# Optimization experiments

Measured on AMD Instinct MI355X. Metric: run time of the kernel, lower is better.

The kernel has to match this reference:

```python
import jax, jax.numpy as jnp
import numpy as np

D = 768
H = 12
DH = 64
S = 1500
SCALE = 0.125  # 1/sqrt(64)


def setup_inputs() -> dict:
    key = jax.random.key(0)
    ks = jax.random.split(key, 8)
    def w(k):
        return jax.random.normal(k, (D, D), dtype=jnp.float32) * (1.0 / np.sqrt(D))
    x = jax.random.normal(ks[0], (8, S, D), dtype=jnp.float32)
    return {
        "x": x,
        "Wq": w(ks[1]), "bq": jax.random.normal(ks[2], (D,), dtype=jnp.float32) * 0.02,
        "Wk": w(ks[3]),
        "Wv": w(ks[4]), "bv": jax.random.normal(ks[5], (D,), dtype=jnp.float32) * 0.02,
        "Wo": w(ks[6]), "bo": jax.random.normal(ks[7], (D,), dtype=jnp.float32) * 0.02,
    }


def reference(x, Wq, bq, Wk, Wv, bv, Wo, bo):
    B = x.shape[0]
    # torch Linear: y = x @ W.T + b
    q = (jnp.einsum('bsd,ed->bse', x, Wq) + bq) * SCALE
    k = jnp.einsum('bsd,ed->bse', x, Wk)
    v = jnp.einsum('bsd,ed->bse', x, Wv) + bv
    # split heads: [B, S, H, DH] -> [B, H, S, DH]
    q = q.reshape(B, S, H, DH).transpose(0, 2, 1, 3)
    k = k.reshape(B, S, H, DH).transpose(0, 2, 1, 3)
    v = v.reshape(B, S, H, DH).transpose(0, 2, 1, 3)
    scores = jnp.einsum('bhqd,bhkd->bhqk', q, k)  # [B, H, S, S]
    probs = jax.nn.softmax(scores, axis=-1)
    ctx = jnp.einsum('bhqk,bhkd->bhqd', probs, v)
    ctx = ctx.transpose(0, 2, 1, 3).reshape(B, S, D)
    return jnp.einsum('bsd,ed->bse', ctx, Wo) + bo
```

## Files before the change

kernel.cpp:

```cpp
#include <hip/hip_runtime.h>
#include <hip/hip_bf16.h>

constexpr int kD  = 768;
constexpr int kH  = 12;
constexpr int kDH = 64;
constexpr int kS  = 1500;
constexpr int kSP = 1504;
constexpr int kB  = 8;
constexpr int kM  = kB * kS;
constexpr float kScale = 0.125f;
constexpr float kScaleL2 = 0.125f * 1.44269504088896f;
constexpr int kPSTR = 72;
constexpr int kNK = kD / 32;

typedef __bf16 bf16;
typedef __bf16 bf16x4 __attribute__((ext_vector_type(4)));
typedef __bf16 bf16x8 __attribute__((ext_vector_type(8)));
typedef float  floatx4 __attribute__((ext_vector_type(4)));

__global__ __launch_bounds__(256) void detect_kernel(const void* __restrict__ xraw,
                                                     int* __restrict__ flag) {
    __shared__ int bad;
    if (threadIdx.x == 0) bad = 0;
    __syncthreads();
    const bf16* xb = (const bf16*)xraw;
    int c = 0;
    for (int k = 0; k < 16; k++) {
        int idx = 2 * (threadIdx.x + 256 * k);
        float v = fabsf((float)xb[idx]);
        if (!(v == 0.0f || (v > 1e-20f && v < 1e6f))) c++;
    }
    atomicAdd(&bad, c);
    __syncthreads();
    if (threadIdx.x == 0) *flag = (bad > 8) ? 1 : 0;
}

__global__ __launch_bounds__(256) void cvt_bf16_kernel(const void* __restrict__ src,
                                                       bf16* __restrict__ dst, int n,
                                                       const int* __restrict__ flag) {
    int i = blockIdx.x * 256 + threadIdx.x;
    if (i < n) {
        if (*flag)
            dst[i] = (bf16)((const float*)src)[i];
        else
            dst[i] = ((const bf16*)src)[i];
    }
}

__global__ __launch_bounds__(256) void cvt_w_kernel(const void* __restrict__ s0,
                                                    const void* __restrict__ s1,
                                                    const void* __restrict__ s2,
                                                    const void* __restrict__ s3,
                                                    bf16* __restrict__ dst, int n,
                                                    const int* __restrict__ flag) {
    const int y = blockIdx.y;
    const void* src = (y == 0) ? s0 : (y == 1) ? s1 : (y == 2) ? s2 : s3;
    bf16* d = dst + (size_t)y * n;
    int i = blockIdx.x * 256 + threadIdx.x;
    if (i < n) {
        if (*flag)
            d[i] = (bf16)((const float*)src)[i];
        else
            d[i] = ((const bf16*)src)[i];
    }
}

__global__ __launch_bounds__(256) void cvt_b_kernel(const void* __restrict__ s0,
                                                    const void* __restrict__ s1,
                                                    const void* __restrict__ s2,
                                                    float* __restrict__ dst, int n,
                                                    const int* __restrict__ flag) {
    const int y = blockIdx.y;
    const void* src = (y == 0) ? s0 : (y == 1) ? s1 : s2;
    float* d = dst + (size_t)y * n;
    int i = blockIdx.x * 256 + threadIdx.x;
    if (i < n) {
        if (*flag)
            d[i] = ((const float*)src)[i];
        else
            d[i] = (float)((const bf16*)src)[i];
    }
}

__global__ __launch_bounds__(256) void zeropad_kernel(bf16* __restrict__ q_ws,
                                                      bf16* __restrict__ k_ws,
                                                      bf16* __restrict__ vt_ws) {
    int t = blockIdx.x * 256 + threadIdx.x;
    if (t < kB * kH * (kSP - kS) * kDH) {
        int bh  = t >> 8;
        int rem = t & 255;
        int s   = kS + (rem >> 6);
        int dh  = rem & 63;
        size_t qi = ((size_t)bh * kSP + s) * kDH + dh;
        q_ws[qi] = (bf16)0.f;
        k_ws[qi] = (bf16)0.f;
        size_t vi = ((size_t)bh * kDH + dh) * kSP + s;
        vt_ws[vi] = (bf16)0.f;
    }
}

__device__ __forceinline__ void async_copy16(const bf16* g, bf16* l) {
    __builtin_amdgcn_global_load_lds(
        (const __attribute__((address_space(1))) void*)g,
        (__attribute__((address_space(3))) void*)l,
        16, 0, 0);
}

#define G_STAGE(KK, SB)                                                         \
    {                                                                           \
        const int k0_ = (KK) * 32;                                              \
        async_copy16(gA + k0_, Asm + (SB) * 4096 + wof);                        \
        async_copy16(gA + (size_t)64 * kD + k0_, Asm + (SB) * 4096 + wof + 2048); \
        async_copy16(gB + k0_, Bsm + (SB) * 4096 + wof);                        \
        async_copy16(gB + (size_t)64 * kD + k0_, Bsm + (SB) * 4096 + wof + 2048); \
    }

#define G_COMPUTE(CB)                                                           \
    {                                                                           \
        const bf16* A_ = Asm + (CB) * 4096;                                     \
        const bf16* B_ = Bsm + (CB) * 4096;                                     \
        bf16x8 af[4], bfr[4];                                                   \
        _Pragma("unroll") for (int i = 0; i < 4; i++)                           \
            af[i] = *(const bf16x8*)(A_ + ((wm + i * 16 + lrow) << 5) + (lq << 3)); \
        _Pragma("unroll") for (int j = 0; j < 4; j++)                           \
            bfr[j] = *(const bf16x8*)(B_ + ((wn + j * 16 + lrow) << 5) + (lq << 3)); \
        _Pragma("unroll") for (int i = 0; i < 4; i++)                           \
            _Pragma("unroll") for (int j = 0; j < 4; j++)                       \
                acc[i][j] = __builtin_amdgcn_mfma_f32_16x16x32_bf16(            \
                    af[i], bfr[j], acc[i][j], 0, 0, 0);                         \
    }

#define G_STEP(KK, CB, SB)                                                      \
    {                                                                           \
        if ((KK) + 3 < kNK) G_STAGE((KK) + 3, SB);                              \
        G_COMPUTE(CB);                                                          \
        if ((KK) + 1 < kNK) {                                                   \
            if ((KK) + 3 < kNK) {                                               \
                asm volatile("s_waitcnt vmcnt(8)" ::: "memory");                \
            } else if ((KK) + 2 < kNK) {                                        \
                asm volatile("s_waitcnt vmcnt(4)" ::: "memory");                \
            } else {                                                            \
                asm volatile("s_waitcnt vmcnt(0)" ::: "memory");                \
            }                                                                   \
            __builtin_amdgcn_s_barrier();                                       \
            __builtin_amdgcn_sched_barrier(0);                                  \
        }                                                                       \
    }

__device__ __forceinline__ void gemm128_qb(const bf16* __restrict__ X,
                                           const bf16* __restrict__ W,
                                           int m0, int n0,
                                           bf16* Asm, bf16* Bsm,
                                           floatx4 acc[4][4]) {
    const int tid  = threadIdx.x;
    const int lane = tid & 63;
    const int w    = tid >> 6;
    const int srow = (w << 4) + (lane >> 2);
    const int scol = (lane & 3) << 3;
    const int lrow = lane & 15;
    const int lq   = lane >> 4;
    const int wm   = (w >> 1) << 6;
    const int wn   = (w & 1) << 6;

    const bf16* gA = X + (size_t)(m0 + srow) * kD + scol;
    const bf16* gB = W + (size_t)(n0 + srow) * kD + scol;
    const int wof = w << 9;

    G_STAGE(0, 0);
    G_STAGE(1, 1);
    G_STAGE(2, 2);
    asm volatile("s_waitcnt vmcnt(8)" ::: "memory");
    __builtin_amdgcn_s_barrier();
    __builtin_amdgcn_sched_barrier(0);

#pragma unroll
    for (int ks = 0; ks < kNK; ks += 4) {
        G_STEP(ks,     0, 3);
        G_STEP(ks + 1, 1, 0);
        G_STEP(ks + 2, 2, 1);
        G_STEP(ks + 3, 3, 2);
    }
}

__global__ __launch_bounds__(256) void qkv_kernel(const bf16* __restrict__ X,
                                                  const bf16* __restrict__ Wq,
                                                  const bf16* __restrict__ Wk,
                                                  const bf16* __restrict__ Wv,
                                                  const float* __restrict__ bq,
                                                  const float* __restrict__ bv,
                                                  bf16* __restrict__ q_ws,
                                                  bf16* __restrict__ k_ws,
                                                  bf16* __restrict__ vt_ws) {
    __shared__ bf16 Asm[4 * 4096];
    __shared__ bf16 Bsm[4 * 4096];

    const int lin = blockIdx.x;
    const int wk  = (lin & 7) * 212 + (lin >> 3);
    if (wk >= 94 * 18) return;
    const int bx  = wk / 18;
    const int r   = wk - bx * 18;
    const int m0  = bx << 7;
    const int mat = r / 6;
    const int n0  = (r % 6) << 7;
    const bf16* W = (mat == 0) ? Wq : (mat == 1) ? Wk : Wv;

    floatx4 acc[4][4] = {};
    gemm128_qb(X, W, m0, n0, Asm, Bsm, acc);

    const int tid  = threadIdx.x;
    const int lane = tid & 63;
    const int w    = tid >> 6;
    const int lrow = lane & 15;
    const int lq   = lane >> 4;
    const int wm   = (w >> 1) << 6;
    const int wn   = (w & 1) << 6;

    if (mat == 2) {
#pragma unroll
        for (int i = 0; i < 4; i++) {
#pragma unroll
            for (int j = 0; j < 4; j++) {
                const int n  = n0 + wn + j * 16 + lrow;
                const int hh = n >> 6, dh = n & 63;
                const float bval = bv[n];
                const int m = m0 + wm + i * 16 + lq * 4;
                if (m >= kM) continue;
                const int bb = m / kS, s = m - bb * kS;
                bf16x4 pv;
#pragma unroll
                for (int r2 = 0; r2 < 4; r2++) pv[r2] = (bf16)(acc[i][j][r2] + bval);
                *(bf16x4*)(vt_ws + (((size_t)(bb * kH + hh)) * kDH + dh) * kSP + s) = pv;
            }
        }
    } else {
        bf16* const dst = (mat == 0) ? q_ws : k_ws;
#pragma unroll
        for (int i = 0; i < 4; i++) {
#pragma unroll
            for (int j = 0; j < 4; j++) {
                const int n  = n0 + wn + j * 16 + lrow;
                const int hh = n >> 6, dh = n & 63;
                const float bval = (mat == 0) ? bq[n] : 0.f;
#pragma unroll
                for (int r2 = 0; r2 < 4; r2++) {
                    const int m = m0 + wm + i * 16 + lq * 4 + r2;
                    if (m >= kM) continue;
                    float v = acc[i][j][r2];
                    if (mat == 0) v = (v + bval) * kScaleL2;
                    const int bb = m / kS, s = m - bb * kS;
                    dst[(((size_t)(bb * kH + hh)) * kSP + s) * kDH + dh] = (bf16)v;
                }
            }
        }
    }
}

__global__ __launch_bounds__(256) void out_kernel(const bf16* __restrict__ X,
                                                  const bf16* __restrict__ Wo,
                                                  const float* __restrict__ bo,
                                                  float* __restrict__ outf) {
    __shared__ bf16 Asm[4 * 4096];
    __shared__ bf16 Bsm[4 * 4096];

    const int lin = blockIdx.x;
    const int xcd = lin & 7;
    const int ii  = lin >> 3;
    constexpr int q = 564 / 8, r = 564 % 8;
    if (xcd >= r && ii >= q) return;
    const int wk = (xcd < r) ? xcd * (q + 1) + ii
                             : r * (q + 1) + (xcd - r) * q + ii;
    const int bx = wk / 6;
    const int m0 = bx << 7;
    const int n0 = (wk - bx * 6) << 7;

    floatx4 acc[4][4] = {};
    gemm128_qb(X, Wo, m0, n0, Asm, Bsm, acc);

    const int tid  = threadIdx.x;
    const int lane = tid & 63;
    const int w    = tid >> 6;
    const int lrow = lane & 15;
    const int lq   = lane >> 4;
    const int wm   = (w >> 1) << 6;
    const int wn   = (w & 1) << 6;

#pragma unroll
    for (int i = 0; i < 4; i++) {
#pragma unroll
        for (int j = 0; j < 4; j++) {
            const int n = n0 + wn + j * 16 + lrow;
            const float bval = bo[n];
#pragma unroll
            for (int r2 = 0; r2 < 4; r2++) {
                const int m = m0 + wm + i * 16 + lq * 4 + r2;
                if (m >= kM) continue;
                outf[(size_t)m * kD + n] = acc[i][j][r2] + bval;
            }
        }
    }
}

__device__ __forceinline__ const bf16* lds_at(const bf16* sm, int row, int cb) {
    return sm + row * 64 + ((cb ^ ((row & 7) << 4)) >> 1);
}

__device__ __forceinline__ void stage_k(const bf16* __restrict__ kbase, int s0,
                                        bf16* ksm, int w, int lane) {
#pragma unroll
    for (int i = 0; i < 2; i++) {
        const int sidx = i * 4 + w;
        const int row  = sidx * 8 + (lane >> 3);
        const int cb   = (lane & 7) << 4;
        const int scb  = cb ^ ((row & 7) << 4);
        int gr = s0 + row;
        if (gr >= kSP) gr = 1472;
        async_copy16(kbase + (size_t)gr * kDH + (scb >> 1), ksm + sidx * 512);
    }
}

__device__ __forceinline__ void stage_v(const bf16* __restrict__ vbase, int s0,
                                        bf16* vsm, int w, int lane) {
#pragma unroll
    for (int i = 0; i < 2; i++) {
        const int sidx = i * 4 + w;
        const int row  = sidx * 8 + (lane >> 3);
        const int cb   = (lane & 7) << 4;
        const int scb  = cb ^ ((row & 7) << 4);
        int key = s0 + (scb >> 1);
        if (key >= kSP) key = 1472;
        async_copy16(vbase + (size_t)row * kSP + key, vsm + sidx * 512);
    }
}

__device__ __forceinline__ void qk_mfma_lds(const bf16* ksm,
                                            const bf16x8 qf[2][2],
                                            floatx4 sc[2][4],
                                            int col, int quad) {
#pragma unroll
    for (int t = 0; t < 4; t++) {
        const int r = 16 * t + col;
        const bf16x8 kf0 = *(const bf16x8*)lds_at(ksm, r, quad * 16);
        const bf16x8 kf1 = *(const bf16x8*)lds_at(ksm, r, 64 + quad * 16);
        __builtin_amdgcn_s_setprio(1);
#pragma unroll
        for (int qt = 0; qt < 2; qt++) {
            floatx4 a = {0.f, 0.f, 0.f, 0.f};
            a = __builtin_amdgcn_mfma_f32_16x16x32_bf16(kf0, qf[qt][0], a, 0, 0, 0);
            a = __builtin_amdgcn_mfma_f32_16x16x32_bf16(kf1, qf[qt][1], a, 0, 0, 0);
            sc[qt][t] = a;
        }
        __builtin_amdgcn_s_setprio(0);
    }
}

template <bool MASK>
__device__ __forceinline__ void exp_store(const floatx4 sc[2][4],
                                          bf16* __restrict__ Pw,
                                          float lsum[2],
                                          int s0, int col, int quad) {
#pragma unroll
    for (int qt = 0; qt < 2; qt++)
#pragma unroll
        for (int t = 0; t < 4; t++) {
            bf16x4 pv;
#pragma unroll
            for (int r = 0; r < 4; r++) {
                float p;
                if (MASK && (s0 + 16 * t + quad * 4 + r >= kS)) {
                    p = 0.f;
                } else {
                    asm("v_exp_f32 %0, %1" : "=v"(p) : "v"(sc[qt][t][r]));
                }
                lsum[qt] += p;
                pv[r] = (bf16)p;
            }
            *(bf16x4*)(Pw + (qt * 16 + col) * kPSTR + 16 * t + quad * 4) = pv;
        }
}

__device__ __forceinline__ void pv_lds(const bf16* vsm,
                                       const bf16* __restrict__ Pr,
                                       floatx4 Oacc[2][4],
                                       int col, int quad) {
    bf16x8 pa[2][2];
#pragma unroll
    for (int qt = 0; qt < 2; qt++)
#pragma unroll
        for (int kc = 0; kc < 2; kc++)
            pa[qt][kc] = *(const bf16x8*)(Pr + (qt * 16 + col) * kPSTR + kc * 32 + quad * 8);
#pragma unroll
    for (int n = 0; n < 4; n++) {
        const int row = n * 16 + col;
#pragma unroll
        for (int kc = 0; kc < 2; kc++) {
            const bf16x8 vf = *(const bf16x8*)lds_at(vsm, row, kc * 64 + quad * 16);
            __builtin_amdgcn_s_setprio(1);
#pragma unroll
            for (int qt = 0; qt < 2; qt++)
                Oacc[qt][n] = __builtin_amdgcn_mfma_f32_16x16x32_bf16(
                    pa[qt][kc], vf, Oacc[qt][n], 0, 0, 0);
            __builtin_amdgcn_s_setprio(0);
        }
    }
}

__global__ __launch_bounds__(256, 2) void fattn_kernel(const bf16* __restrict__ q_ws,
                                                       const bf16* __restrict__ k_ws,
                                                       const bf16* __restrict__ vt_ws,
                                                       bf16* __restrict__ ctx) {
    __shared__ bf16 Ksm[2][64 * 64];
    __shared__ bf16 Vsm[2][64 * 64];
    __shared__ bf16 Pbuf[4][32 * kPSTR];

    const int idx = blockIdx.x;
    const int bh  = idx % 96;
    const int qb  = idx / 96;
    const int b   = bh / kH;
    const int h   = bh - b * kH;
    const int tid  = threadIdx.x;
    const int w    = tid >> 6;
    const int lane = tid & 63;
    const int col  = lane & 15;
    const int quad = lane >> 4;
    const int q0   = qb * 128 + w * 32;
    const bool active = (q0 < kS);

    const bf16* qbase = q_ws  + (size_t)bh * kSP * kDH;
    const bf16* kbase = k_ws  + (size_t)bh * kSP * kDH;
    const bf16* vbase = vt_ws + (size_t)bh * kDH * kSP;

    bf16x8 qf[2][2] = {};
    if (active) {
#pragma unroll
        for (int qt = 0; qt < 2; qt++) {
            const bf16* qr = qbase + (size_t)(q0 + qt * 16 + col) * kDH + quad * 8;
            qf[qt][0] = *(const bf16x8*)(qr);
            qf[qt][1] = *(const bf16x8*)(qr + 32);
        }
    }

    float lsum[2] = {0.f, 0.f};
    floatx4 Oacc[2][4];
#pragma unroll
    for (int qt = 0; qt < 2; qt++)
#pragma unroll
        for (int n = 0; n < 4; n++) Oacc[qt][n] = (floatx4){0.f, 0.f, 0.f, 0.f};

    bf16* const P = &Pbuf[w][0];
    floatx4 sc[2][4];

    stage_k(kbase, 0, &Ksm[0][0], w, lane);
    stage_v(vbase, 0, &Vsm[0][0], w, lane);
    __syncthreads();

    int buf = 0;
    for (int c = 0; c < 23; ++c) {
        stage_k(kbase, (c + 1) * 64, &Ksm[buf ^ 1][0], w, lane);
        stage_v(vbase, (c + 1) * 64, &Vsm[buf ^ 1][0], w, lane);
        if (active) {
            qk_mfma_lds(&Ksm[buf][0], qf, sc, col, quad);
            exp_store<false>(sc, P, lsum, c * 64, col, quad);
            pv_lds(&Vsm[buf][0], P, Oacc, col, quad);
        }
        __syncthreads();
        buf ^= 1;
    }
    if (active) {
        qk_mfma_lds(&Ksm[buf][0], qf, sc, col, quad);
        exp_store<true>(sc, P, lsum, 1472, col, quad);
        pv_lds(&Vsm[buf][0], P, Oacc, col, quad);

#pragma unroll
        for (int qt = 0; qt < 2; qt++) {
            float l = lsum[qt];
            l += __shfl_xor(l, 16);
            l += __shfl_xor(l, 32);
            const float rinv_col = 1.0f / l;
            float ri[4];
#pragma unroll
            for (int r = 0; r < 4; r++)
                ri[r] = __shfl(rinv_col, quad * 4 + r, 16);
#pragma unroll
            for (int n = 0; n < 4; n++)
#pragma unroll
                for (int r = 0; r < 4; r++) {
                    const int q = q0 + qt * 16 + quad * 4 + r;
                    if (q < kS)
                        ctx[((size_t)(b * kS + q)) * kD + h * kDH + n * 16 + col] =
                            (bf16)(Oacc[qt][n][r] * ri[r]);
                }
        }
    }
}

extern "C" void kernel_launch(void* const* d_in, const int* in_sizes, int n_in,
                              void* d_out, int out_size, void* d_ws, size_t ws_size,
                              hipStream_t stream) {
    float* out_f = (float*)d_out;

    constexpr size_t nX = (size_t)kM * kD;
    constexpr size_t nW = (size_t)kD * kD;
    constexpr size_t per_qkv = (size_t)kB * kH * kSP * kDH;

    bf16* xb    = (bf16*)d_ws;
    bf16* Wqb   = xb + nX;
    bf16* Wkb   = Wqb + nW;
    bf16* Wvb   = Wkb + nW;
    bf16* Wob   = Wvb + nW;
    bf16* q_ws  = Wob + nW;
    bf16* k_ws  = q_ws + per_qkv;
    bf16* vt_ws = k_ws + per_qkv;
    float* bqf  = (float*)(vt_ws + per_qkv);
    float* bvf  = bqf + kD;
    float* bof  = bvf + kD;
    int*  flag  = (int*)(bof + kD);
    bf16* ctx   = xb;

    detect_kernel<<<1, 256, 0, stream>>>(d_in[0], flag);
    cvt_bf16_kernel<<<(int)((nX + 255) / 256), 256, 0, stream>>>(d_in[0], xb, (int)nX, flag);
    cvt_w_kernel<<<dim3((int)((nW + 255) / 256), 4), 256, 0, stream>>>(
        d_in[1], d_in[3], d_in[4], d_in[6], Wqb, (int)nW, flag);
    cvt_b_kernel<<<dim3(3, 3), 256, 0, stream>>>(
        d_in[2], d_in[5], d_in[7], bqf, kD, flag);

    zeropad_kernel<<<96, 256, 0, stream>>>(q_ws, k_ws, vt_ws);
    qkv_kernel<<<dim3(1696), 256, 0, stream>>>(xb, Wqb, Wkb, Wvb, bqf, bvf,
                                               q_ws, k_ws, vt_ws);

    fattn_kernel<<<dim3(12 * 96), 256, 0, stream>>>(q_ws, k_ws, vt_ws, ctx);

    out_kernel<<<dim3(568), 256, 0, stream>>>(ctx, Wob, bof, out_f);
}
```

Baseline: 328.7 us.

## Triple-buffer K/V tiles in flash attention with partial vmcnt waits

Switches the attention kernel's K/V shared-memory staging from double to triple buffering, prefetching two tiles ahead. The full __syncthreads is replaced by a partial s_waitcnt vmcnt plus a raw s_barrier, so loads for the next tile can still be in flight while the current tile is computed. This is meant to hide global-load latency better. It raises LDS use, which may reduce occupancy at 2 blocks per CU, and it relies on the exact count of loads issued by stage_k and stage_v matching vmcnt(4).

```diff
diff --git a/kernel.cpp b/kernel.cpp
--- a/kernel.cpp
+++ b/kernel.cpp
@@ -408,8 +408,8 @@
                                                        const bf16* __restrict__ k_ws,
                                                        const bf16* __restrict__ vt_ws,
                                                        bf16* __restrict__ ctx) {
-    __shared__ bf16 Ksm[2][64 * 64];
-    __shared__ bf16 Vsm[2][64 * 64];
+    __shared__ bf16 Ksm[3][64 * 64];
+    __shared__ bf16 Vsm[3][64 * 64];
     __shared__ bf16 Pbuf[4][32 * kPSTR];
 
     const int idx = blockIdx.x;
@@ -451,24 +451,36 @@
 
     stage_k(kbase, 0, &Ksm[0][0], w, lane);
     stage_v(vbase, 0, &Vsm[0][0], w, lane);
-    __syncthreads();
-
-    int buf = 0;
+    stage_k(kbase, 64, &Ksm[1][0], w, lane);
+    stage_v(vbase, 64, &Vsm[1][0], w, lane);
+    asm volatile("s_waitcnt vmcnt(4)" ::: "memory");
+    __builtin_amdgcn_s_barrier();
+    __builtin_amdgcn_sched_barrier(0);
+
     for (int c = 0; c < 23; ++c) {
-        stage_k(kbase, (c + 1) * 64, &Ksm[buf ^ 1][0], w, lane);
-        stage_v(vbase, (c + 1) * 64, &Vsm[buf ^ 1][0], w, lane);
+        if (c + 2 < 24) {
+            const int b2 = (c + 2) % 3;
+            stage_k(kbase, (c + 2) * 64, &Ksm[b2][0], w, lane);
+            stage_v(vbase, (c + 2) * 64, &Vsm[b2][0], w, lane);
+        }
+        const int bc = c % 3;
         if (active) {
-            qk_mfma_lds(&Ksm[buf][0], qf, sc, col, quad);
+            qk_mfma_lds(&Ksm[bc][0], qf, sc, col, quad);
             exp_store<false>(sc, P, lsum, c * 64, col, quad);
-            pv_lds(&Vsm[buf][0], P, Oacc, col, quad);
-        }
-        __syncthreads();
-        buf ^= 1;
+            pv_lds(&Vsm[bc][0], P, Oacc, col, quad);
+        }
+        if (c + 2 < 24) {
+            asm volatile("s_waitcnt vmcnt(4)" ::: "memory");
+        } else {
+            asm volatile("s_waitcnt vmcnt(0)" ::: "memory");
+        }
+        __builtin_amdgcn_s_barrier();
+        __builtin_amdgcn_sched_barrier(0);
     }
     if (active) {
-        qk_mfma_lds(&Ksm[buf][0], qf, sc, col, quad);
+        qk_mfma_lds(&Ksm[2][0], qf, sc, col, quad);
         exp_store<true>(sc, P, lsum, 1472, col, quad);
-        pv_lds(&Vsm[buf][0], P, Oacc, col, quad);
+        pv_lds(&Vsm[2][0], P, Oacc, col, quad);
 
 #pragma unroll
         for (int qt = 0; qt < 2; qt++) {
```

Measured after the change: 355.6 us. 8.2% more time.
